# Performance work log

Hardware: AMD Instinct MI355X
Metric: run time of the kernel (lower is better)

Reference implementation:

```python
import jax, jax.numpy as jnp
import numpy as np
import math

SCOPE = 27
RICKER_WIDTH = 4.0
DAMP = 0.12
IN_CHANNELS = 128
BATCH, H, W = 64, 64, 64


def _mexican_hat(scope, std, damping):
    # Ricker (mexican hat) wavelet sampled on integer grid centered at scope//2,
    # matching weight_initialization.mexican_hat(scope, std, damping).
    x = np.arange(scope, dtype=np.float32) - scope // 2
    a = 2.0 / (np.sqrt(3.0 * std) * np.pi ** 0.25)
    wavelet = a * (1.0 - (x / std) ** 2) * np.exp(-(x ** 2) / (2.0 * std ** 2))
    return (damping * wavelet).astype(np.float32)


def setup_inputs() -> dict:
    key = jax.random.key(0)
    activations = jax.random.normal(key, (BATCH, IN_CHANNELS, H, W), dtype=jnp.float32)
    inhibition_filter = jnp.asarray(_mexican_hat(SCOPE, RICKER_WIDTH, DAMP)).reshape(1, 1, SCOPE)
    return {"activations": activations, "inhibition_filter": inhibition_filter}


def reference(activations, inhibition_filter):
    # activations: (N, C, H, W); inhibition_filter: (1, 1, scope)
    C = activations.shape[1]
    scope = inhibition_filter.shape[-1]

    # pad_roll: zero-pad filter to length C, roll so center lands at index 0 side
    pad_left = (C - scope) // 2
    pad_right = C - scope - pad_left
    k = jnp.concatenate([
        jnp.zeros((pad_left,), dtype=inhibition_filter.dtype),
        inhibition_filter[0, 0],
        jnp.zeros((pad_right,), dtype=inhibition_filter.dtype),
    ])
    k = jnp.roll(k, C // 2 + 1)  # (C,)

    # kronecker delta along channels
    delta = jnp.zeros((C,), dtype=activations.dtype).at[0].set(1.0)

    # frequency-domain deconvolution along the channel axis
    Fk = jnp.fft.fft(delta - k)  # (C,) complex
    sig = jnp.transpose(activations, (0, 2, 3, 1))  # NCHW -> NHWC
    out = jnp.fft.ifft(jnp.fft.fft(sig, axis=-1) / Fk, axis=-1).real
    return jnp.transpose(out, (0, 3, 1, 2)).astype(activations.dtype)
```

## Files before the change

### kernel.cpp

```cpp
#include <hip/hip_runtime.h>


typedef short bf16x8 __attribute__((ext_vector_type(8)));
typedef float f32x4 __attribute__((ext_vector_type(4)));

#define MFMA16x16x32 __builtin_amdgcn_mfma_f32_16x16x32_bf16

__device__ __forceinline__ unsigned short f2bf(float f) {
  union { float f; unsigned u; } v; v.f = f;
  unsigned u = v.u;
  u += 0x7fffu + ((u >> 16) & 1u);
  return (unsigned short)(u >> 16);
}

__global__ void build_g(const float* __restrict__ filt, float* __restrict__ g) {
  __shared__ float ct[128], st[128], fr[128], fi[128];
  const int t = threadIdx.x;
  const float ang = (float)t * 0.049087385212340526f;
  float s, c;
  __sincosf(ang, &s, &c);
  ct[t] = c; st[t] = s;
  __syncthreads();

  float re = 1.f, im = 0.f;
  for (int tt = 0; tt < 27; ++tt) {
    const int j = (115 + tt) & 127;
    const int idx = (j * t) & 127;
    const float kv = filt[tt];
    re -= kv * ct[idx];
    im += kv * st[idx];
  }
  fr[t] = re; fi[t] = im;
  __syncthreads();

  float acc = 0.f;
  for (int m = 0; m < 128; ++m) {
    const int idx = (m * t) & 127;
    const float dr = fr[m], di = fi[m];
    acc += (ct[idx] * dr + st[idx] * di) / (dr * dr + di * di);
  }
  g[t] = acc * (1.0f / 128.0f);
}

__global__ __launch_bounds__(256) void conv_inhib(
    const float* __restrict__ X, const float* __restrict__ gtab,
    float* __restrict__ Y) {
  __shared__ __align__(16) unsigned short Xt[128 * 136];
  __shared__ float gs[128];

  const int tid = threadIdx.x;
  const int l = tid & 63;
  const int w = tid >> 6;
  const int lane15 = l & 15;
  const int quad = l >> 4;

  const int bid = blockIdx.x;
  const int nimg = bid >> 5;
  const int s0 = (bid & 31) << 7;
  const float* Xn = X + (size_t)nimg * (128 * 4096);
  float* Yn = Y + (size_t)nimg * (128 * 4096);

  if (tid < 128) gs[tid] = gtab[tid];

  {
    const int ssub = (tid & 31) << 2;
    const int cbase = tid >> 5;
#pragma unroll
    for (int r = 0; r < 16; ++r) {
      const int c = cbase + (r << 3);
      const float4 v = *(const float4*)(Xn + (size_t)c * 4096 + s0 + ssub);
      unsigned short* dst = &Xt[c];
      dst[(ssub + 0) * 136] = f2bf(v.x);
      dst[(ssub + 1) * 136] = f2bf(v.y);
      dst[(ssub + 2) * 136] = f2bf(v.z);
      dst[(ssub + 3) * 136] = f2bf(v.w);
    }
  }
  __syncthreads();

  bf16x8 afrag[2][4];
#pragma unroll
  for (int i = 0; i < 2; ++i) {
    const int m = (w << 5) + (i << 4) + lane15;
#pragma unroll
    for (int kk = 0; kk < 4; ++kk) {
      const int kbase = (kk << 5) + (quad << 3);
#pragma unroll
      for (int j = 0; j < 8; ++j) {
        afrag[i][kk][j] = (short)f2bf(gs[(m - (kbase + j)) & 127]);
      }
    }
  }

  f32x4 acc[2][8];
#pragma unroll
  for (int i = 0; i < 2; ++i)
#pragma unroll
    for (int ns = 0; ns < 8; ++ns)
      acc[i][ns] = (f32x4){0.f, 0.f, 0.f, 0.f};

#pragma unroll
  for (int ns = 0; ns < 8; ++ns) {
    const int srow = (ns << 4) + lane15;
#pragma unroll
    for (int kk = 0; kk < 4; ++kk) {
      const bf16x8 b = *(const bf16x8*)&Xt[srow * 136 + (kk << 5) + (quad << 3)];
      acc[0][ns] = MFMA16x16x32(afrag[0][kk], b, acc[0][ns], 0, 0, 0);
      acc[1][ns] = MFMA16x16x32(afrag[1][kk], b, acc[1][ns], 0, 0, 0);
    }
  }

#pragma unroll
  for (int i = 0; i < 2; ++i) {
#pragma unroll
    for (int r = 0; r < 4; ++r) {
      const int c = (w << 5) + (i << 4) + (quad << 2) + r;
      float* Yc = Yn + (size_t)c * 4096 + s0 + lane15;
#pragma unroll
      for (int ns = 0; ns < 8; ++ns) {
        Yc[ns << 4] = acc[i][ns][r];
      }
    }
  }
}

extern "C" void kernel_launch(void* const* d_in, const int* in_sizes, int n_in,
                              void* d_out, int out_size, void* d_ws, size_t ws_size,
                              hipStream_t stream) {
  const float* act = (const float*)d_in[0];
  const float* filt = (const float*)d_in[1];
  float* out = (float*)d_out;
  float* g = (float*)d_ws;

  build_g<<<1, 128, 0, stream>>>(filt, g);
  conv_inhib<<<2048, 256, 0, stream>>>(act, g, out);
}
```

Before: 246.5 us.

## Swap MFMA operand roles, swizzle LDS layout, vectorize staging and output stores

Swaps the GEMM operand roles so the activation tile becomes the A operand and the circulant filter matrix the B operand. The accumulator layout then lets each lane write contiguous float4 outputs instead of scalar strided stores. The LDS transpose now packs 8 channels per lane into 16-byte writes with an XOR swizzle in place of padding. The filter table is precomputed in bf16 and a launch-bounds occupancy hint is added. The aim is fewer, wider LDS and global memory transactions, at the cost of more registers held live during the load phase.

```diff
diff --git a/kernel.cpp b/kernel.cpp
--- a/kernel.cpp
+++ b/kernel.cpp
@@ -6,14 +6,15 @@
 
 #define MFMA16x16x32 __builtin_amdgcn_mfma_f32_16x16x32_bf16
 
-__device__ __forceinline__ unsigned short f2bf(float f) {
+__device__ __forceinline__ unsigned short f2bf_rne(float f) {
   union { float f; unsigned u; } v; v.f = f;
   unsigned u = v.u;
   u += 0x7fffu + ((u >> 16) & 1u);
   return (unsigned short)(u >> 16);
 }
 
-__global__ void build_g(const float* __restrict__ filt, float* __restrict__ g) {
+__global__ void build_g(const float* __restrict__ filt,
+                        unsigned short* __restrict__ gbf) {
   __shared__ float ct[128], st[128], fr[128], fi[128];
   const int t = threadIdx.x;
   const float ang = (float)t * 0.049087385212340526f;
@@ -39,14 +40,14 @@
     const float dr = fr[m], di = fi[m];
     acc += (ct[idx] * dr + st[idx] * di) / (dr * dr + di * di);
   }
-  g[t] = acc * (1.0f / 128.0f);
+  gbf[t] = f2bf_rne(acc * (1.0f / 128.0f));
 }
 
-__global__ __launch_bounds__(256) void conv_inhib(
-    const float* __restrict__ X, const float* __restrict__ gtab,
+__global__ __launch_bounds__(256, 4) void conv_inhib(
+    const float* __restrict__ X, const unsigned short* __restrict__ gtab,
     float* __restrict__ Y) {
-  __shared__ __align__(16) unsigned short Xt[128 * 136];
-  __shared__ float gs[128];
+  __shared__ __align__(16) unsigned short Xt[128 * 128];
+  __shared__ unsigned short gsh[128];
 
   const int tid = threadIdx.x;
   const int l = tid & 63;
@@ -60,66 +61,73 @@
   const float* Xn = X + (size_t)nimg * (128 * 4096);
   float* Yn = Y + (size_t)nimg * (128 * 4096);
 
-  if (tid < 128) gs[tid] = gtab[tid];
+  if (tid < 128) gsh[tid] = gtab[tid];
 
   {
-    const int ssub = (tid & 31) << 2;
-    const int cbase = tid >> 5;
+    const int cb = tid & 7;
+    const int sg = tid >> 3;
+    const float* src = Xn + (size_t)(cb << 3) * 4096 + s0 + (sg << 2);
+    f32x4 v[16];
 #pragma unroll
-    for (int r = 0; r < 16; ++r) {
-      const int c = cbase + (r << 3);
-      const float4 v = *(const float4*)(Xn + (size_t)c * 4096 + s0 + ssub);
-      unsigned short* dst = &Xt[c];
-      dst[(ssub + 0) * 136] = f2bf(v.x);
-      dst[(ssub + 1) * 136] = f2bf(v.y);
-      dst[(ssub + 2) * 136] = f2bf(v.z);
-      dst[(ssub + 3) * 136] = f2bf(v.w);
+    for (int p = 0; p < 2; ++p)
+#pragma unroll
+      for (int i = 0; i < 8; ++i)
+        v[(p << 3) + i] = *(const f32x4*)(src + (size_t)((p << 6) + i) * 4096);
+#pragma unroll
+    for (int p = 0; p < 2; ++p) {
+      const int chunk = cb + (p << 3);
+#pragma unroll
+      for (int j = 0; j < 4; ++j) {
+        const int s = (sg << 2) + j;
+        bf16x8 t;
+#pragma unroll
+        for (int i = 0; i < 8; ++i) t[i] = (short)f2bf_rne(v[(p << 3) + i][j]);
+        *(bf16x8*)&Xt[(s << 7) + ((chunk ^ (s & 7)) << 3)] = t;
+      }
     }
   }
   __syncthreads();
 
-  bf16x8 afrag[2][4];
+  bf16x8 bfrag[2][4];
 #pragma unroll
-  for (int i = 0; i < 2; ++i) {
-    const int m = (w << 5) + (i << 4) + lane15;
+  for (int nt = 0; nt < 2; ++nt) {
+    const int cout = (w << 5) + (nt << 4) + lane15;
 #pragma unroll
     for (int kk = 0; kk < 4; ++kk) {
-      const int kbase = (kk << 5) + (quad << 3);
+      const int kb = (kk << 5) + (quad << 3);
 #pragma unroll
-      for (int j = 0; j < 8; ++j) {
-        afrag[i][kk][j] = (short)f2bf(gs[(m - (kbase + j)) & 127]);
-      }
+      for (int j = 0; j < 8; ++j)
+        bfrag[nt][kk][j] = (short)gsh[(cout - kb - j) & 127];
     }
   }
 
-  f32x4 acc[2][8];
+  f32x4 acc[8][2];
 #pragma unroll
-  for (int i = 0; i < 2; ++i)
+  for (int mt = 0; mt < 8; ++mt)
 #pragma unroll
-    for (int ns = 0; ns < 8; ++ns)
-      acc[i][ns] = (f32x4){0.f, 0.f, 0.f, 0.f};
+    for (int nt = 0; nt < 2; ++nt)
+      acc[mt][nt] = (f32x4){0.f, 0.f, 0.f, 0.f};
 
 #pragma unroll
-  for (int ns = 0; ns < 8; ++ns) {
-    const int srow = (ns << 4) + lane15;
+  for (int mt = 0; mt < 8; ++mt) {
+    const int srow = (mt << 4) + lane15;
+    const int rb = srow << 7;
+    const int sx = srow & 7;
 #pragma unroll
     for (int kk = 0; kk < 4; ++kk) {
-      const bf16x8 b = *(const bf16x8*)&Xt[srow * 136 + (kk << 5) + (quad << 3)];
-      acc[0][ns] = MFMA16x16x32(afrag[0][kk], b, acc[0][ns], 0, 0, 0);
-      acc[1][ns] = MFMA16x16x32(afrag[1][kk], b, acc[1][ns], 0, 0, 0);
+      const bf16x8 a = *(const bf16x8*)&Xt[rb + ((((kk << 2) + quad) ^ sx) << 3)];
+      acc[mt][0] = MFMA16x16x32(a, bfrag[0][kk], acc[mt][0], 0, 0, 0);
+      acc[mt][1] = MFMA16x16x32(a, bfrag[1][kk], acc[mt][1], 0, 0, 0);
     }
   }
 
 #pragma unroll
-  for (int i = 0; i < 2; ++i) {
+  for (int nt = 0; nt < 2; ++nt) {
+    const int c = (w << 5) + (nt << 4) + lane15;
+    float* Yc = Yn + (size_t)c * 4096 + s0 + (quad << 2);
 #pragma unroll
-    for (int r = 0; r < 4; ++r) {
-      const int c = (w << 5) + (i << 4) + (quad << 2) + r;
-      float* Yc = Yn + (size_t)c * 4096 + s0 + lane15;
-#pragma unroll
-      for (int ns = 0; ns < 8; ++ns) {
-        Yc[ns << 4] = acc[i][ns][r];
-      }
+    for (int mt = 0; mt < 8; ++mt) {
+      *(f32x4*)(Yc + (mt << 4)) = acc[mt][nt];
     }
   }
 }
@@ -130,7 +138,7 @@
   const float* act = (const float*)d_in[0];
   const float* filt = (const float*)d_in[1];
   float* out = (float*)d_out;
-  float* g = (float*)d_ws;
+  unsigned short* g = (unsigned short*)d_ws;
 
   build_g<<<1, 128, 0, stream>>>(filt, g);
   conv_inhib<<<2048, 256, 0, stream>>>(act, g, out);
```

After: 246.5 us. Within noise of the previous version (-0.0%).
